# Kernel optimization log

Measured on AMD Instinct MI355X. Metric: run time of the kernel, lower is better.

The kernel has to match this reference:

```python
import jax, jax.numpy as jnp
import numpy as np

SEGMENTS = 64
SU2NDIM = 16
N = 16  # SU(2^4) matrix dimension
BATCH = 128


def setup_inputs() -> dict:
    key = jax.random.key(0)
    # Small scale keeps expm well-conditioned (skew-ish generators in practice)
    x = 0.1 * jax.random.normal(key, (BATCH, SEGMENTS * SU2NDIM, N, N), dtype=jnp.float32)
    return {"x": x}


def _batched_expm(a):
    # a: [..., N, N] -> expm over last two dims
    flat = a.reshape((-1, N, N))
    ex = jax.vmap(jax.scipy.linalg.expm)(flat)
    return ex.reshape(a.shape)


def reference(x):
    # maintensor = expm(-x), reversed along axis 0 (faithful to source)
    m = _batched_expm(-x)            # [B, S*D, N, N]
    m = m[::-1]                      # tf.reverse(maintensor, [0])
    b = m.shape[0]
    # tf.split along axis 1 into SEGMENTS contiguous chunks of SU2NDIM
    m = m.reshape(b, SEGMENTS, SU2NDIM, N, N)
    # Sequential chain product per segment: U = M[D-1] @ ... @ M[1] @ M[0] @ I
    ms = jnp.moveaxis(m, 2, 0)       # [D, B, S, N, N]
    u0 = jnp.broadcast_to(jnp.eye(N, dtype=x.dtype), (b, SEGMENTS, N, N))
    def step(u, mj):
        return mj @ u, None
    u, _ = jax.lax.scan(step, u0, ms)
    return u                         # [B, SEGMENTS, N, N] == transpose([1,0,2,3]) of stacked list
```

## Files before the change

kernel.cpp:

```cpp
#include <hip/hip_runtime.h>

typedef float f32x4 __attribute__((ext_vector_type(4)));
typedef short s16x8 __attribute__((ext_vector_type(8)));
typedef unsigned int uint;
typedef uint u32x4 __attribute__((ext_vector_type(4)));

union Frag {
  u32x4 u;
  s16x8 s;
};

__device__ __forceinline__ uint pack_bf16(float f0, float f1) {
  uint a = __float_as_uint(f0) + 0x8000u;
  uint b = __float_as_uint(f1) + 0x8000u;
  return __builtin_amdgcn_perm(b, a, 0x07060302u);
}

#define LGKM0() __asm__ __volatile__("s_waitcnt lgkmcnt(0)" ::: "memory")

__device__ __forceinline__ f32x4 expm_neg(const float* __restrict__ A,
                                          uint* __restrict__ bf, int lo, int g,
                                          int gl, bool low, f32x4 idm,
                                          Frag c7I) {
  f32x4 r0 = *(const f32x4*)(A + lo * 16 + 8 * gl);
  f32x4 r1 = *(const f32x4*)(A + lo * 16 + 8 * gl + 4);
  Frag xa;
  xa.u[0] = low ? pack_bf16(r0[0], r0[1]) : 0u;
  xa.u[1] = low ? pack_bf16(r0[2], r0[3]) : 0u;
  xa.u[2] = low ? pack_bf16(r1[0], r1[1]) : 0u;
  xa.u[3] = low ? pack_bf16(r1[2], r1[3]) : 0u;

  f32x4 acc = idm * (1.f / 720.f);
  f32x4 t = __builtin_amdgcn_mfma_f32_16x16x32_bf16(xa.s, c7I.s, acc, 0, 0, 0);

  const float SK[6] = {-1.f / 120.f, 1.f / 24.f, -1.f / 6.f, 0.5f, -1.f, 1.f};
#pragma unroll
  for (int kk = 0; kk < 6; ++kk) {
    bf[lo * 8 + 2 * g] = pack_bf16(t[0], t[1]);
    bf[lo * 8 + 2 * g + 1] = pack_bf16(t[2], t[3]);
    LGKM0();
    Frag tb;
    tb.u = *(const u32x4*)&bf[lo * 8 + 4 * gl];
    acc = idm * SK[kk];
    t = __builtin_amdgcn_mfma_f32_16x16x32_bf16(xa.s, tb.s, acc, 0, 0, 0);
  }
  return t;
}

__global__ __launch_bounds__(256, 8) void unitary_kernel(
    const float* __restrict__ x, float* __restrict__ out) {
  __shared__ uint BfS[4][128];
  __shared__ float EfS[4][256];

  const int tid = threadIdx.x;
  const int w = tid >> 6;
  const int l = tid & 63;
  const int lo = l & 15;
  const int g = l >> 4;
  const int gl = g & 1;
  const bool low = (g < 2);

  uint* bf = BfS[w];
  float* ef = EfS[w];

  const int ch = blockIdx.x * 4 + w;
  const int bi = ch >> 6;
  const int s = ch & 63;
  const float* xb = x + ((size_t)(127 - bi) * 1024 + (size_t)s * 16) * 256;

  f32x4 idm;
  idm[0] = (4 * g + 0 == lo) ? 1.f : 0.f;
  idm[1] = (4 * g + 1 == lo) ? 1.f : 0.f;
  idm[2] = (4 * g + 2 == lo) ? 1.f : 0.f;
  idm[3] = (4 * g + 3 == lo) ? 1.f : 0.f;

  Frag c7I;
  {
    uint c7b = pack_bf16(-1.f / 5040.f, 0.f) & 0xFFFFu;
    int jd = lo - 8 * gl;
    uint val = c7b << (16 * (jd & 1));
    c7I.u[0] = (low && jd >= 0 && (jd >> 1) == 0) ? val : 0u;
    c7I.u[1] = (low && jd >= 0 && (jd >> 1) == 1) ? val : 0u;
    c7I.u[2] = (low && jd >= 0 && (jd >> 1) == 2) ? val : 0u;
    c7I.u[3] = (low && jd >= 0 && (jd >> 1) == 3) ? val : 0u;
  }

  f32x4 uc = expm_neg(xb, bf, lo, g, gl, low, idm, c7I);

  for (int j = 1; j < 16; ++j) {
    f32x4 e = expm_neg(xb + (size_t)j * 256, bf, lo, g, gl, low, idm, c7I);
    ef[(4 * g + 0) * 16 + lo] = e[0];
    ef[(4 * g + 1) * 16 + lo] = e[1];
    ef[(4 * g + 2) * 16 + lo] = e[2];
    ef[(4 * g + 3) * 16 + lo] = e[3];
    bf[lo * 8 + 2 * g] = pack_bf16(uc[0], uc[1]);
    bf[lo * 8 + 2 * g + 1] = pack_bf16(uc[2], uc[3]);
    LGKM0();
    f32x4 q0 = *(const f32x4*)&ef[lo * 16 + 8 * gl];
    f32x4 q1 = *(const f32x4*)&ef[lo * 16 + 8 * gl + 4];
    Frag ea;
    ea.u[0] = low ? pack_bf16(q0[0], q0[1]) : 0u;
    ea.u[1] = low ? pack_bf16(q0[2], q0[3]) : 0u;
    ea.u[2] = low ? pack_bf16(q1[0], q1[1]) : 0u;
    ea.u[3] = low ? pack_bf16(q1[2], q1[3]) : 0u;
    Frag ub;
    ub.u = *(const u32x4*)&bf[lo * 8 + 4 * gl];
    f32x4 z = {0.f, 0.f, 0.f, 0.f};
    uc = __builtin_amdgcn_mfma_f32_16x16x32_bf16(ea.s, ub.s, z, 0, 0, 0);
  }

  float* op = out + (size_t)ch * 256;
  op[(4 * g + 0) * 16 + lo] = uc[0];
  op[(4 * g + 1) * 16 + lo] = uc[1];
  op[(4 * g + 2) * 16 + lo] = uc[2];
  op[(4 * g + 3) * 16 + lo] = uc[3];
}

extern "C" void kernel_launch(void* const* d_in, const int* in_sizes, int n_in,
                              void* d_out, int out_size, void* d_ws,
                              size_t ws_size, hipStream_t stream) {
  const float* x = (const float*)d_in[0];
  float* out = (float*)d_out;
  unitary_kernel<<<dim3(2048), dim3(256), 0, stream>>>(x, out);
}
```

Baseline: 191.3 us.

## Use split bf16 hi/lo products and a shortened Horner expm in the chain

Operands are split into bf16 high and low parts and packed into the K=32 MFMA slots, so each product recovers near-fp32 accuracy: the exponential uses hi/lo of x, and the chain product uses two MFMAs over the hi/lo parts. The Horner polynomial now starts from an fp32 FMA seed, which removes one MFMA step, and the transposed x load fills the A fragment directly. The explicit lgkmcnt waits are replaced with compiler-only fences and the shared-memory layouts are padded. This adds split arithmetic and an extra MFMA per chain step, and it relies on the compiler to order LDS accesses correctly.

Result: no change. 190.6 us (-0.3%).

```diff
diff --git a/kernel.cpp b/kernel.cpp
--- a/kernel.cpp
+++ b/kernel.cpp
@@ -10,38 +10,53 @@
   s16x8 s;
 };
 
-__device__ __forceinline__ uint pack_bf16(float f0, float f1) {
+__device__ __forceinline__ uint packhi(float f0, float f1) {
   uint a = __float_as_uint(f0) + 0x8000u;
   uint b = __float_as_uint(f1) + 0x8000u;
   return __builtin_amdgcn_perm(b, a, 0x07060302u);
 }
 
-#define LGKM0() __asm__ __volatile__("s_waitcnt lgkmcnt(0)" ::: "memory")
+__device__ __forceinline__ void split2(float f0, float f1, uint& hi, uint& lo) {
+  uint a0 = __float_as_uint(f0) + 0x8000u;
+  uint a1 = __float_as_uint(f1) + 0x8000u;
+  hi = __builtin_amdgcn_perm(a1, a0, 0x07060302u);
+  float h0 = __uint_as_float(a0 & 0xFFFF0000u);
+  float h1 = __uint_as_float(a1 & 0xFFFF0000u);
+  lo = packhi(f0 - h0, f1 - h1);
+}
 
-__device__ __forceinline__ f32x4 expm_neg(const float* __restrict__ A,
-                                          uint* __restrict__ bf, int lo, int g,
-                                          int gl, bool low, f32x4 idm,
-                                          Frag c7I) {
-  f32x4 r0 = *(const f32x4*)(A + lo * 16 + 8 * gl);
-  f32x4 r1 = *(const f32x4*)(A + lo * 16 + 8 * gl + 4);
+#define CFENCE() __asm__ __volatile__("" ::: "memory")
+
+__device__ __forceinline__ f32x4 expm_negT(const float* __restrict__ A,
+                                           uint* __restrict__ hb, int lo,
+                                           int g, int gt, bool low, f32x4 idm) {
+  float c0 = A[(8 * gt + 0) * 16 + lo], c1 = A[(8 * gt + 1) * 16 + lo];
+  float c2 = A[(8 * gt + 2) * 16 + lo], c3 = A[(8 * gt + 3) * 16 + lo];
+  float c4 = A[(8 * gt + 4) * 16 + lo], c5 = A[(8 * gt + 5) * 16 + lo];
+  float c6 = A[(8 * gt + 6) * 16 + lo], c7 = A[(8 * gt + 7) * 16 + lo];
+  f32x4 xr = *(const f32x4*)(A + lo * 16 + 4 * g);
+  uint h, lw;
   Frag xa;
-  xa.u[0] = low ? pack_bf16(r0[0], r0[1]) : 0u;
-  xa.u[1] = low ? pack_bf16(r0[2], r0[3]) : 0u;
-  xa.u[2] = low ? pack_bf16(r1[0], r1[1]) : 0u;
-  xa.u[3] = low ? pack_bf16(r1[2], r1[3]) : 0u;
-
-  f32x4 acc = idm * (1.f / 720.f);
-  f32x4 t = __builtin_amdgcn_mfma_f32_16x16x32_bf16(xa.s, c7I.s, acc, 0, 0, 0);
-
-  const float SK[6] = {-1.f / 120.f, 1.f / 24.f, -1.f / 6.f, 0.5f, -1.f, 1.f};
+  split2(c0, c1, h, lw); xa.u[0] = low ? h : lw;
+  split2(c2, c3, h, lw); xa.u[1] = low ? h : lw;
+  split2(c4, c5, h, lw); xa.u[2] = low ? h : lw;
+  split2(c6, c7, h, lw); xa.u[3] = low ? h : lw;
+  f32x4 t;
 #pragma unroll
-  for (int kk = 0; kk < 6; ++kk) {
-    bf[lo * 8 + 2 * g] = pack_bf16(t[0], t[1]);
-    bf[lo * 8 + 2 * g + 1] = pack_bf16(t[2], t[3]);
-    LGKM0();
+  for (int i = 0; i < 4; ++i)
+    t[i] = fmaf(1.f / 720.f, xr[i], (-1.f / 120.f) * idm[i]);
+  const float SK[5] = {1.f / 24.f, -1.f / 6.f, 0.5f, -1.f, 1.f};
+  uint* wp = hb + lo * 12 + 2 * g;
+  const uint* rp = hb + lo * 12 + 4 * gt;
+#pragma unroll
+  for (int k = 0; k < 5; ++k) {
+    wp[0] = packhi(t[0], t[1]);
+    wp[1] = packhi(t[2], t[3]);
+    CFENCE();
     Frag tb;
-    tb.u = *(const u32x4*)&bf[lo * 8 + 4 * gl];
-    acc = idm * SK[kk];
+    tb.u = *(const u32x4*)rp;
+    CFENCE();
+    f32x4 acc = idm * SK[k];
     t = __builtin_amdgcn_mfma_f32_16x16x32_bf16(xa.s, tb.s, acc, 0, 0, 0);
   }
   return t;
@@ -49,24 +64,25 @@
 
 __global__ __launch_bounds__(256, 8) void unitary_kernel(
     const float* __restrict__ x, float* __restrict__ out) {
-  __shared__ uint BfS[4][128];
-  __shared__ float EfS[4][256];
+  __shared__ uint HB[4][192];
+  __shared__ uint PE[4][320];
+  __shared__ uint PU[4][320];
 
   const int tid = threadIdx.x;
   const int w = tid >> 6;
   const int l = tid & 63;
   const int lo = l & 15;
   const int g = l >> 4;
-  const int gl = g & 1;
-  const bool low = (g < 2);
+  const int gt = g & 1;
+  const bool low = g < 2;
 
-  uint* bf = BfS[w];
-  float* ef = EfS[w];
+  uint* hb = HB[w];
+  uint* pe = PE[w];
+  uint* pu = PU[w];
 
   const int ch = blockIdx.x * 4 + w;
-  const int bi = ch >> 6;
-  const int s = ch & 63;
-  const float* xb = x + ((size_t)(127 - bi) * 1024 + (size_t)s * 16) * 256;
+  const float* xb =
+      x + ((size_t)(127 - (ch >> 6)) * 1024 + (size_t)(ch & 63) * 16) * 256;
 
   f32x4 idm;
   idm[0] = (4 * g + 0 == lo) ? 1.f : 0.f;
@@ -74,39 +90,58 @@
   idm[2] = (4 * g + 2 == lo) ? 1.f : 0.f;
   idm[3] = (4 * g + 3 == lo) ? 1.f : 0.f;
 
-  Frag c7I;
+  Frag ifr;
   {
-    uint c7b = pack_bf16(-1.f / 5040.f, 0.f) & 0xFFFFu;
-    int jd = lo - 8 * gl;
-    uint val = c7b << (16 * (jd & 1));
-    c7I.u[0] = (low && jd >= 0 && (jd >> 1) == 0) ? val : 0u;
-    c7I.u[1] = (low && jd >= 0 && (jd >> 1) == 1) ? val : 0u;
-    c7I.u[2] = (low && jd >= 0 && (jd >> 1) == 2) ? val : 0u;
-    c7I.u[3] = (low && jd >= 0 && (jd >> 1) == 3) ? val : 0u;
+    uint v = ((lo >> 3) == gt) ? (0x3F80u << (16 * (lo & 1))) : 0u;
+    int slot = (lo >> 1) & 3;
+    ifr.u[0] = (slot == 0) ? v : 0u;
+    ifr.u[1] = (slot == 1) ? v : 0u;
+    ifr.u[2] = (slot == 2) ? v : 0u;
+    ifr.u[3] = (slot == 3) ? v : 0u;
   }
 
-  f32x4 uc = expm_neg(xb, bf, lo, g, gl, low, idm, c7I);
+  uint* pew = pe + lo * 20 + 4 * g;
+  const uint* pea = pe + lo * 20 + 8 * gt + (low ? 0 : 2);
+  uint* puw = pu + lo * 20 + 4 * g;
+  const uint* pub = pu + lo * 20 + 8 * gt;
 
-  for (int j = 1; j < 16; ++j) {
-    f32x4 e = expm_neg(xb + (size_t)j * 256, bf, lo, g, gl, low, idm, c7I);
-    ef[(4 * g + 0) * 16 + lo] = e[0];
-    ef[(4 * g + 1) * 16 + lo] = e[1];
-    ef[(4 * g + 2) * 16 + lo] = e[2];
-    ef[(4 * g + 3) * 16 + lo] = e[3];
-    bf[lo * 8 + 2 * g] = pack_bf16(uc[0], uc[1]);
-    bf[lo * 8 + 2 * g + 1] = pack_bf16(uc[2], uc[3]);
-    LGKM0();
-    f32x4 q0 = *(const f32x4*)&ef[lo * 16 + 8 * gl];
-    f32x4 q1 = *(const f32x4*)&ef[lo * 16 + 8 * gl + 4];
+  f32x4 uc;
+#pragma unroll 1
+  for (int j = 0; j < 16; ++j) {
+    f32x4 et = expm_negT(xb + j * 256, hb, lo, g, gt, low, idm);
+    uint h0, l0, h1, l1;
+    split2(et[0], et[1], h0, l0);
+    split2(et[2], et[3], h1, l1);
+    *(u32x4*)pew = (u32x4){h0, h1, l0, l1};
+    if (j) {
+      split2(uc[0], uc[1], h0, l0);
+      split2(uc[2], uc[3], h1, l1);
+      *(u32x4*)puw = (u32x4){h0, h1, l0, l1};
+    }
+    CFENCE();
     Frag ea;
-    ea.u[0] = low ? pack_bf16(q0[0], q0[1]) : 0u;
-    ea.u[1] = low ? pack_bf16(q0[2], q0[3]) : 0u;
-    ea.u[2] = low ? pack_bf16(q1[0], q1[1]) : 0u;
-    ea.u[3] = low ? pack_bf16(q1[2], q1[3]) : 0u;
-    Frag ub;
-    ub.u = *(const u32x4*)&bf[lo * 8 + 4 * gl];
+    ea.u[0] = pea[0];
+    ea.u[1] = pea[1];
+    ea.u[2] = pea[4];
+    ea.u[3] = pea[5];
     f32x4 z = {0.f, 0.f, 0.f, 0.f};
-    uc = __builtin_amdgcn_mfma_f32_16x16x32_bf16(ea.s, ub.s, z, 0, 0, 0);
+    if (j) {
+      Frag b1, b2;
+      b1.u[0] = pub[0];
+      b1.u[1] = pub[1];
+      b1.u[2] = pub[4];
+      b1.u[3] = pub[5];
+      b2.u[0] = pub[2];
+      b2.u[1] = pub[3];
+      b2.u[2] = pub[6];
+      b2.u[3] = pub[7];
+      CFENCE();
+      f32x4 t1 = __builtin_amdgcn_mfma_f32_16x16x32_bf16(ea.s, b1.s, z, 0, 0, 0);
+      uc = __builtin_amdgcn_mfma_f32_16x16x32_bf16(ea.s, b2.s, t1, 0, 0, 0);
+    } else {
+      CFENCE();
+      uc = __builtin_amdgcn_mfma_f32_16x16x32_bf16(ea.s, ifr.s, z, 0, 0, 0);
+    }
   }
 
   float* op = out + (size_t)ch * 256;
```

## Switch expm to fp16 MFMA with register-resident Horner and split-fp16 chain products

Applied to the files above, without the earlier changes.

Replaces the bf16 16x16x32 MFMA path with fp16 16x16x16 MFMAs, whose B-operand layout matches the accumulator layout. This lets the Taylor Horner steps convert the accumulator in registers instead of going through LDS each step. Two expm matrices are processed together to interleave their independent MFMA chains. The chain product uses a hi/lo fp16 split with three MFMAs to recover accuracy, and the LDS transpose buffer is padded to stride 20 to avoid bank conflicts. It adds MFMA work in the chain and drops the explicit lgkmcnt waits in favour of compiler fences, relying on wave-local LDS ordering.

New measurement: 192.6 us. About the same (+0.7%).

```diff
diff --git a/kernel.cpp b/kernel.cpp
--- a/kernel.cpp
+++ b/kernel.cpp
@@ -1,72 +1,47 @@
 #include <hip/hip_runtime.h>
 
 typedef float f32x4 __attribute__((ext_vector_type(4)));
-typedef short s16x8 __attribute__((ext_vector_type(8)));
-typedef unsigned int uint;
-typedef uint u32x4 __attribute__((ext_vector_type(4)));
+typedef _Float16 f16x2 __attribute__((ext_vector_type(2)));
+typedef _Float16 f16x4 __attribute__((ext_vector_type(4)));
 
-union Frag {
-  u32x4 u;
-  s16x8 s;
+union H4 {
+  f16x4 v;
+  f16x2 p[2];
 };
 
-__device__ __forceinline__ uint pack_bf16(float f0, float f1) {
-  uint a = __float_as_uint(f0) + 0x8000u;
-  uint b = __float_as_uint(f1) + 0x8000u;
-  return __builtin_amdgcn_perm(b, a, 0x07060302u);
+#define CFENCE() __asm__ __volatile__("" ::: "memory")
+
+__device__ __forceinline__ void split4(f32x4 e, H4& hi, H4& lw) {
+  _Float16 h0 = (_Float16)e[0], h1 = (_Float16)e[1];
+  _Float16 h2 = (_Float16)e[2], h3 = (_Float16)e[3];
+  hi.v = (f16x4){h0, h1, h2, h3};
+  lw.v = (f16x4){(_Float16)(e[0] - (float)h0), (_Float16)(e[1] - (float)h1),
+                 (_Float16)(e[2] - (float)h2), (_Float16)(e[3] - (float)h3)};
 }
 
-#define LGKM0() __asm__ __volatile__("s_waitcnt lgkmcnt(0)" ::: "memory")
-
-__device__ __forceinline__ f32x4 expm_neg(const float* __restrict__ A,
-                                          uint* __restrict__ bf, int lo, int g,
-                                          int gl, bool low, f32x4 idm,
-                                          Frag c7I) {
-  f32x4 r0 = *(const f32x4*)(A + lo * 16 + 8 * gl);
-  f32x4 r1 = *(const f32x4*)(A + lo * 16 + 8 * gl + 4);
-  Frag xa;
-  xa.u[0] = low ? pack_bf16(r0[0], r0[1]) : 0u;
-  xa.u[1] = low ? pack_bf16(r0[2], r0[3]) : 0u;
-  xa.u[2] = low ? pack_bf16(r1[0], r1[1]) : 0u;
-  xa.u[3] = low ? pack_bf16(r1[2], r1[3]) : 0u;
-
-  f32x4 acc = idm * (1.f / 720.f);
-  f32x4 t = __builtin_amdgcn_mfma_f32_16x16x32_bf16(xa.s, c7I.s, acc, 0, 0, 0);
-
-  const float SK[6] = {-1.f / 120.f, 1.f / 24.f, -1.f / 6.f, 0.5f, -1.f, 1.f};
-#pragma unroll
-  for (int kk = 0; kk < 6; ++kk) {
-    bf[lo * 8 + 2 * g] = pack_bf16(t[0], t[1]);
-    bf[lo * 8 + 2 * g + 1] = pack_bf16(t[2], t[3]);
-    LGKM0();
-    Frag tb;
-    tb.u = *(const u32x4*)&bf[lo * 8 + 4 * gl];
-    acc = idm * SK[kk];
-    t = __builtin_amdgcn_mfma_f32_16x16x32_bf16(xa.s, tb.s, acc, 0, 0, 0);
-  }
-  return t;
+__device__ __forceinline__ void chain_step(f32x4& uc, const H4& eh,
+                                           const H4& el) {
+  H4 uh, ul;
+  split4(uc, uh, ul);
+  f32x4 z = {0.f, 0.f, 0.f, 0.f};
+  f32x4 a = __builtin_amdgcn_mfma_f32_16x16x16f16(eh.v, ul.v, z, 0, 0, 0);
+  a = __builtin_amdgcn_mfma_f32_16x16x16f16(el.v, uh.v, a, 0, 0, 0);
+  uc = __builtin_amdgcn_mfma_f32_16x16x16f16(eh.v, uh.v, a, 0, 0, 0);
 }
 
 __global__ __launch_bounds__(256, 8) void unitary_kernel(
     const float* __restrict__ x, float* __restrict__ out) {
-  __shared__ uint BfS[4][128];
-  __shared__ float EfS[4][256];
+  __shared__ float EF[4][2][16 * 20];
 
   const int tid = threadIdx.x;
   const int w = tid >> 6;
   const int l = tid & 63;
   const int lo = l & 15;
   const int g = l >> 4;
-  const int gl = g & 1;
-  const bool low = (g < 2);
-
-  uint* bf = BfS[w];
-  float* ef = EfS[w];
 
   const int ch = blockIdx.x * 4 + w;
-  const int bi = ch >> 6;
-  const int s = ch & 63;
-  const float* xb = x + ((size_t)(127 - bi) * 1024 + (size_t)s * 16) * 256;
+  const float* xb =
+      x + ((size_t)(127 - (ch >> 6)) * 1024 + (size_t)(ch & 63) * 16) * 256;
 
   f32x4 idm;
   idm[0] = (4 * g + 0 == lo) ? 1.f : 0.f;
@@ -74,39 +49,59 @@
   idm[2] = (4 * g + 2 == lo) ? 1.f : 0.f;
   idm[3] = (4 * g + 3 == lo) ? 1.f : 0.f;
 
-  Frag c7I;
-  {
-    uint c7b = pack_bf16(-1.f / 5040.f, 0.f) & 0xFFFFu;
-    int jd = lo - 8 * gl;
-    uint val = c7b << (16 * (jd & 1));
-    c7I.u[0] = (low && jd >= 0 && (jd >> 1) == 0) ? val : 0u;
-    c7I.u[1] = (low && jd >= 0 && (jd >> 1) == 1) ? val : 0u;
-    c7I.u[2] = (low && jd >= 0 && (jd >> 1) == 2) ? val : 0u;
-    c7I.u[3] = (low && jd >= 0 && (jd >> 1) == 3) ? val : 0u;
-  }
+  float* ef0 = &EF[w][0][0];
+  float* ef1 = &EF[w][1][0];
 
-  f32x4 uc = expm_neg(xb, bf, lo, g, gl, low, idm, c7I);
+  const float SK[6] = {-1.f / 120.f, 1.f / 24.f, -1.f / 6.f, 0.5f, -1.f, 1.f};
 
-  for (int j = 1; j < 16; ++j) {
-    f32x4 e = expm_neg(xb + (size_t)j * 256, bf, lo, g, gl, low, idm, c7I);
-    ef[(4 * g + 0) * 16 + lo] = e[0];
-    ef[(4 * g + 1) * 16 + lo] = e[1];
-    ef[(4 * g + 2) * 16 + lo] = e[2];
-    ef[(4 * g + 3) * 16 + lo] = e[3];
-    bf[lo * 8 + 2 * g] = pack_bf16(uc[0], uc[1]);
-    bf[lo * 8 + 2 * g + 1] = pack_bf16(uc[2], uc[3]);
-    LGKM0();
-    f32x4 q0 = *(const f32x4*)&ef[lo * 16 + 8 * gl];
-    f32x4 q1 = *(const f32x4*)&ef[lo * 16 + 8 * gl + 4];
-    Frag ea;
-    ea.u[0] = low ? pack_bf16(q0[0], q0[1]) : 0u;
-    ea.u[1] = low ? pack_bf16(q0[2], q0[3]) : 0u;
-    ea.u[2] = low ? pack_bf16(q1[0], q1[1]) : 0u;
-    ea.u[3] = low ? pack_bf16(q1[2], q1[3]) : 0u;
-    Frag ub;
-    ub.u = *(const u32x4*)&bf[lo * 8 + 4 * gl];
-    f32x4 z = {0.f, 0.f, 0.f, 0.f};
-    uc = __builtin_amdgcn_mfma_f32_16x16x32_bf16(ea.s, ub.s, z, 0, 0, 0);
+  f32x4 uc;
+
+#pragma unroll 1
+  for (int grp = 0; grp < 8; ++grp) {
+    const float* A0 = xb + (size_t)(2 * grp) * 256;
+    const float* A1 = A0 + 256;
+    f32x4 x0 = *(const f32x4*)(A0 + lo * 16 + 4 * g);
+    f32x4 x1 = *(const f32x4*)(A1 + lo * 16 + 4 * g);
+    H4 xa0, xa1;
+    xa0.v = (f16x4){(_Float16)x0[0], (_Float16)x0[1], (_Float16)x0[2],
+                    (_Float16)x0[3]};
+    xa1.v = (f16x4){(_Float16)x1[0], (_Float16)x1[1], (_Float16)x1[2],
+                    (_Float16)x1[3]};
+
+    f32x4 t0 = idm * (1.f / 720.f);
+    f32x4 t1 = t0;
+#pragma unroll
+    for (int k = 0; k < 6; ++k) {
+      H4 b0, b1;
+      b0.v = (f16x4){(_Float16)t0[0], (_Float16)t0[1], (_Float16)t0[2],
+                     (_Float16)t0[3]};
+      b1.v = (f16x4){(_Float16)t1[0], (_Float16)t1[1], (_Float16)t1[2],
+                     (_Float16)t1[3]};
+      f32x4 a0 = idm * SK[k];
+      f32x4 a1 = idm * SK[k];
+      t0 = __builtin_amdgcn_mfma_f32_16x16x16f16(xa0.v, b0.v, a0, 0, 0, 0);
+      t1 = __builtin_amdgcn_mfma_f32_16x16x16f16(xa1.v, b1.v, a1, 0, 0, 0);
+    }
+#pragma unroll
+    for (int i = 0; i < 4; ++i) {
+      ef0[(4 * g + i) * 20 + lo] = t0[i];
+      ef1[(4 * g + i) * 20 + lo] = t1[i];
+    }
+    CFENCE();
+    f32x4 er0 = *(const f32x4*)&ef0[lo * 20 + 4 * g];
+    f32x4 er1 = *(const f32x4*)&ef1[lo * 20 + 4 * g];
+    CFENCE();
+    H4 eh1, el1;
+    split4(er1, eh1, el1);
+    if (grp == 0) {
+      uc = t0;
+      chain_step(uc, eh1, el1);
+    } else {
+      H4 eh0, el0;
+      split4(er0, eh0, el0);
+      chain_step(uc, eh0, el0);
+      chain_step(uc, eh1, el1);
+    }
   }
 
   float* op = out + (size_t)ch * 256;
```
